# Optimization experiments

Hardware: AMD Instinct MI355X
Metric: run time of the kernel (lower is better)

The kernel has to match this reference:

```python
import jax, jax.numpy as jnp
import numpy as np

MODEL_DIM = 1024
N_HEADS = 16
HEAD_DIM = 64  # q_dim == k_dim == v_dim


def setup_inputs() -> dict:
    key = jax.random.key(0)
    ks = jax.random.split(key, 7)
    B, S = 4, 2048
    scale = 1.0 / np.sqrt(MODEL_DIM)
    return {
        "q": jax.random.normal(ks[0], (B, S, MODEL_DIM), dtype=jnp.float32),
        "k": jax.random.normal(ks[1], (B, S, MODEL_DIM), dtype=jnp.float32),
        "v": jax.random.normal(ks[2], (B, S, MODEL_DIM), dtype=jnp.float32),
        # Linear weights stored as [out, in] like torch; no biases.
        "wq": jax.random.normal(ks[3], (N_HEADS * HEAD_DIM, MODEL_DIM), dtype=jnp.float32) * scale,
        "wk": jax.random.normal(ks[4], (N_HEADS * HEAD_DIM, MODEL_DIM), dtype=jnp.float32) * scale,
        "wv": jax.random.normal(ks[5], (N_HEADS * HEAD_DIM, MODEL_DIM), dtype=jnp.float32) * scale,
        "wo": jax.random.normal(ks[6], (MODEL_DIM, N_HEADS * HEAD_DIM), dtype=jnp.float32) * scale,
    }


def reference(q, k, v, wq, wk, wv, wo):
    B, Sq, _ = q.shape
    Sk = k.shape[1]
    # projections: [B,S,D] @ W^T -> [B,S,H*dh] -> [B,H,S,dh]
    qh = (q @ wq.T).reshape(B, Sq, N_HEADS, HEAD_DIM).transpose(0, 2, 1, 3)
    kh = (k @ wk.T).reshape(B, Sk, N_HEADS, HEAD_DIM).transpose(0, 2, 1, 3)
    vh = (v @ wv.T).reshape(B, Sk, N_HEADS, HEAD_DIM).transpose(0, 2, 1, 3)
    # scores [B,H,Sq,Sk], scaled by sqrt(k_dim)
    scores = jnp.einsum('bhqd,bhkd->bhqk', qh, kh) / jnp.sqrt(jnp.float32(HEAD_DIM))
    attn = jax.nn.softmax(scores, axis=-1)
    ctx = jnp.einsum('bhqk,bhkd->bhqd', attn, vh)  # [B,H,Sq,dh]
    ctx = ctx.transpose(0, 2, 1, 3).reshape(B, Sq, N_HEADS * HEAD_DIM)
    return ctx @ wo.T
```

## Files before the change

### kernel.cpp

```cpp
#include <hip/hip_runtime.h>
#include <cstdint>
#include <cstddef>


typedef _Float16 f16x8 __attribute__((ext_vector_type(8)));
typedef _Float16 f16x4 __attribute__((ext_vector_type(4)));
typedef _Float16 f16x2 __attribute__((ext_vector_type(2)));
typedef __fp16 h16x2 __attribute__((ext_vector_type(2)));
typedef float f32x4 __attribute__((ext_vector_type(4)));
typedef float f32x16 __attribute__((ext_vector_type(16)));
typedef unsigned u32x4 __attribute__((ext_vector_type(4)));
typedef int i32x2 __attribute__((ext_vector_type(2)));

#define LDS_CAST(p) ((__attribute__((address_space(3))) void*)(p))
#define GLB_CAST(p) ((const __attribute__((address_space(1))) void*)(p))

__device__ __forceinline__ void gload_lds16(const void* g, void* l) {
  __builtin_amdgcn_global_load_lds(GLB_CAST(g), LDS_CAST(l), 16, 0, 0);
}

__device__ __forceinline__ float fexp2(float x) {
#if __has_builtin(__builtin_amdgcn_exp2f)
  return __builtin_amdgcn_exp2f(x);
#else
  return exp2f(x);
#endif
}

__device__ __forceinline__ f16x2 pkrtz(float a, float b) {
  h16x2 r = __builtin_amdgcn_cvt_pkrtz(a, b);
  return __builtin_bit_cast(f16x2, r);
}

__device__ __forceinline__ float dot2acc(f16x2 a, float acc) {
#if __has_builtin(__builtin_amdgcn_fdot2)
  const f16x2 one2 = {(_Float16)1.0f, (_Float16)1.0f};
  return __builtin_amdgcn_fdot2(a, one2, acc, false);
#else
  return acc + (float)a[0] + (float)a[1];
#endif
}

__device__ __forceinline__ void pl32swap(unsigned& a, unsigned& b) {
#if __has_builtin(__builtin_amdgcn_permlane32_swap)
  i32x2 r = __builtin_amdgcn_permlane32_swap((int)a, (int)b, false, false);
  a = (unsigned)r[0];
  b = (unsigned)r[1];
#else
  asm("v_permlane32_swap_b32 %0, %1" : "+v"(a), "+v"(b));
#endif
}

__global__ void cvt_all(const float* __restrict__ q, const float* __restrict__ k,
                        const float* __restrict__ v, const float* __restrict__ wq,
                        const float* __restrict__ wk, const float* __restrict__ wv,
                        const float* __restrict__ wo, _Float16* __restrict__ oq,
                        _Float16* __restrict__ ok, _Float16* __restrict__ ov,
                        _Float16* __restrict__ owq, _Float16* __restrict__ owk,
                        _Float16* __restrict__ owv, _Float16* __restrict__ owo) {
  int id = blockIdx.x;
  const float* in;
  _Float16* out;
  int base;
  if (id < 24576) {
    int z = id >> 13;
    base = (id & 8191) * 256;
    in = z == 0 ? q : z == 1 ? k : v;
    out = z == 0 ? oq : z == 1 ? ok : ov;
  } else {
    int id2 = id - 24576;
    int z = id2 >> 10;
    base = (id2 & 1023) * 256;
    in = z == 0 ? wq : z == 1 ? wk : z == 2 ? wv : wo;
    out = z == 0 ? owq : z == 1 ? owk : z == 2 ? owv : owo;
  }
  int i = base + threadIdx.x;
  float4 vv = ((const float4*)in)[i];
  f16x4 o = {(_Float16)vv.x, (_Float16)vv.y, (_Float16)vv.z, (_Float16)vv.w};
  ((f16x4*)out)[i] = o;
}

template <int MODE>
__device__ __forceinline__ void gemm_core(const _Float16* __restrict__ A,
                                          const _Float16* __restrict__ W,
                                          void* __restrict__ C, float scale,
                                          _Float16* As, _Float16* Bs) {
  constexpr int K = 1024, N = 1024;
  const int tid = threadIdx.x;
  const int wid = tid >> 6;
  const int lane = tid & 63;
  const int quad = lane >> 4;
  const int l16 = lane & 15;
  const int wm = wid >> 1;
  const int wn = wid & 1;

  int lin = blockIdx.y * 8 + blockIdx.x;
  int swz = (lin & 7) * 64 + (lin >> 3);
  const int m0 = (swz >> 3) * 128;
  const int n0 = (swz & 7) * 128;

  const _Float16* Ag = A + (size_t)m0 * K;
  const _Float16* Bg = W + (size_t)n0 * K;

  f32x4 acc[4][4];
#pragma unroll
  for (int i = 0; i < 4; i++)
#pragma unroll
    for (int j = 0; j < 4; j++) acc[i][j] = (f32x4){0.f, 0.f, 0.f, 0.f};

  const int lrow = lane >> 2;
  const int swsrc = ((lane & 3) ^ ((lane >> 3) & 3)) * 8;

  auto stage = [&](_Float16* Ad, _Float16* Bd, int k0) {
#pragma unroll
    for (int i = 0; i < 2; i++) {
      int issue = wid * 2 + i;
      gload_lds16(Ag + (size_t)(issue * 16 + lrow) * K + k0 + swsrc,
                  Ad + issue * 512);
      gload_lds16(Bg + (size_t)(issue * 16 + lrow) * K + k0 + swsrc,
                  Bd + issue * 512);
    }
  };

  const int swq = (quad ^ ((l16 >> 1) & 3)) * 8;

  auto compute = [&](const _Float16* Ab, const _Float16* Bb) {
    f16x8 af[4], bfr[4];
#pragma unroll
    for (int mt = 0; mt < 4; mt++)
      af[mt] = *(const f16x8*)&Ab[(wm * 64 + mt * 16 + l16) * 32 + swq];
#pragma unroll
    for (int nt = 0; nt < 4; nt++)
      bfr[nt] = *(const f16x8*)&Bb[(wn * 64 + nt * 16 + l16) * 32 + swq];
#pragma unroll
    for (int mt = 0; mt < 4; mt++)
#pragma unroll
      for (int nt = 0; nt < 4; nt++)
        acc[mt][nt] = __builtin_amdgcn_mfma_f32_16x16x32_f16(
            af[mt], bfr[nt], acc[mt][nt], 0, 0, 0);
  };

  _Float16* A0 = As;
  _Float16* A1 = As + 4096;
  _Float16* A2 = As + 8192;
  _Float16* B0 = Bs;
  _Float16* B1 = Bs + 4096;
  _Float16* B2 = Bs + 8192;

  stage(A0, B0, 0);
  for (int g = 0; g < 10; g++) {
    int t3 = g * 3;
    stage(A1, B1, (t3 + 1) * 32);
    asm volatile("s_waitcnt vmcnt(4)" ::: "memory");
    __builtin_amdgcn_s_barrier();
    asm volatile("" ::: "memory");
    compute(A0, B0);
    stage(A2, B2, (t3 + 2) * 32);
    asm volatile("s_waitcnt vmcnt(4)" ::: "memory");
    __builtin_amdgcn_s_barrier();
    asm volatile("" ::: "memory");
    compute(A1, B1);
    stage(A0, B0, (t3 + 3) * 32);
    asm volatile("s_waitcnt vmcnt(4)" ::: "memory");
    __builtin_amdgcn_s_barrier();
    asm volatile("" ::: "memory");
    compute(A2, B2);
  }
  stage(A1, B1, 31 * 32);
  asm volatile("s_waitcnt vmcnt(4)" ::: "memory");
  __builtin_amdgcn_s_barrier();
  asm volatile("" ::: "memory");
  compute(A0, B0);
  asm volatile("s_waitcnt vmcnt(0)" ::: "memory");
  __builtin_amdgcn_s_barrier();
  asm volatile("" ::: "memory");
  compute(A1, B1);

#pragma unroll
  for (int mt = 0; mt < 4; mt++) {
#pragma unroll
    for (int nt = 0; nt < 4; nt++) {
#pragma unroll
      for (int r = 0; r < 4; r++) {
        int m = m0 + wm * 64 + mt * 16 + quad * 4 + r;
        int n = n0 + wn * 64 + nt * 16 + l16;
        float v = acc[mt][nt][r] * scale;
        if (MODE == 0) {
          ((float*)C)[(size_t)m * N + n] = v;
        } else {
          int b = m >> 11, s = m & 2047;
          int h = n >> 6, dd = n & 63;
          size_t bh = (size_t)(b * 16 + h);
          if (MODE == 1) {
            ((_Float16*)C)[(bh * 2048 + s) * 64 + dd] = (_Float16)v;
          } else if (MODE == 3) {
            int kt2 = s >> 5, l32k = s & 31;
            int s4 = dd >> 4, hi8 = (dd >> 3) & 1, j = dd & 7;
            size_t idx = (bh * 32 + (kt2 >> 1)) * 8192 +
                         (((kt2 & 1) * 4 + s4) * 512) + (hi8 * 32 + l32k) * 8 +
                         j;
            ((_Float16*)C)[idx] = (_Float16)v;
          } else {
            int kt = s >> 6, ks = (s >> 4) & 3, hi8 = (s >> 3) & 1, j = s & 7;
            int dt = dd >> 5, l32v = dd & 31;
            size_t idx = (bh * 32 + kt) * 8192 + 4096 + ((dt * 4 + ks) * 512) +
                         (hi8 * 32 + l32v) * 8 + j;
            ((_Float16*)C)[idx] = (_Float16)v;
          }
        }
      }
    }
  }
}

__global__ __launch_bounds__(256, 3) void gemm_qkv(
    const _Float16* __restrict__ qb, const _Float16* __restrict__ kb,
    const _Float16* __restrict__ vb, const _Float16* __restrict__ wq,
    const _Float16* __restrict__ wk, const _Float16* __restrict__ wv,
    _Float16* __restrict__ Qh, _Float16* __restrict__ KVf) {
  __shared__ _Float16 As[3 * 128 * 32];
  __shared__ _Float16 Bs[3 * 128 * 32];
  if (blockIdx.z == 0)
    gemm_core<1>(qb, wq, Qh, 0.18033688f, As, Bs);
  else if (blockIdx.z == 1)
    gemm_core<3>(kb, wk, KVf, 1.0f, As, Bs);
  else
    gemm_core<4>(vb, wv, KVf, 1.0f, As, Bs);
}

__global__ __launch_bounds__(256, 3) void gemm_wo(
    const _Float16* __restrict__ ctx, const _Float16* __restrict__ wo,
    float* __restrict__ out) {
  __shared__ _Float16 As[3 * 128 * 32];
  __shared__ _Float16 Bs[3 * 128 * 32];
  gemm_core<0>(ctx, wo, out, 1.0f, As, Bs);
}

__global__ __launch_bounds__(512, 2) void attn_kernel(
    const _Float16* __restrict__ Qh, const _Float16* __restrict__ KVf,
    _Float16* __restrict__ ctx) {
  __shared__ _Float16 sKV[3][8192];

  const int qt = blockIdx.x;
  const int bh = blockIdx.y;
  const int tid = threadIdx.x;
  const int wid = tid >> 6;
  const int lane = tid & 63;
  const int l32 = lane & 31;
  const int hi = lane >> 5;

  const _Float16* Qg = Qh + ((size_t)bh * 2048 + qt * 256 + wid * 32) * 64;
  const _Float16* KVb = KVf + (size_t)bh * 262144;

  f16x8 aq[4];
#pragma unroll
  for (int s = 0; s < 4; s++)
    aq[s] = *(const f16x8*)(Qg + (size_t)l32 * 64 + s * 16 + hi * 8);

  f32x16 acc[2];
#pragma unroll
  for (int i = 0; i < 16; i++) {
    acc[0][i] = 0.f;
    acc[1][i] = 0.f;
  }
  float lsA = 0.f, lsB = 0.f;

  auto stage = [&](int buf, int kt) {
    const _Float16* t = KVb + (size_t)kt * 8192;
#pragma unroll
    for (int i = 0; i < 2; i++) {
      int c = wid * 2 + i;
      gload_lds16(t + c * 512 + lane * 8, &sKV[buf][c * 512]);
    }
  };

  auto body = [&](const _Float16* Ks) {
    const _Float16* Vs = Ks + 4096;
    f16x8 kf0[4], kf1[4];
#pragma unroll
    for (int s = 0; s < 4; s++) {
      kf0[s] = *(const f16x8*)&Ks[(0 * 4 + s) * 512 + lane * 8];
      kf1[s] = *(const f16x8*)&Ks[(4 + s) * 512 + lane * 8];
    }

    f32x16 s0, s1;
#pragma unroll
    for (int i = 0; i < 16; i++) {
      s0[i] = 0.f;
      s1[i] = 0.f;
    }
#pragma unroll
    for (int s = 0; s < 4; s++) {
      s0 = __builtin_amdgcn_mfma_f32_32x32x16_f16(kf0[s], aq[s], s0, 0, 0, 0);
      s1 = __builtin_amdgcn_mfma_f32_32x32x16_f16(kf1[s], aq[s], s1, 0, 0, 0);
    }

    f16x8 vf0[4], vf1[4];
#pragma unroll
    for (int g = 0; g < 4; g++) {
      vf0[g] = *(const f16x8*)&Vs[(0 * 4 + g) * 512 + lane * 8];
      vf1[g] = *(const f16x8*)&Vs[(4 + g) * 512 + lane * 8];
    }

    unsigned hw[2][8];
#pragma unroll
    for (int i = 0; i < 8; i++) {
      f16x2 hh = pkrtz(fexp2(s0[2 * i]), fexp2(s0[2 * i + 1]));
      if (i & 1)
        lsB = dot2acc(hh, lsB);
      else
        lsA = dot2acc(hh, lsA);
      hw[0][i] = __builtin_bit_cast(unsigned, hh);
    }
#pragma unroll
    for (int i = 0; i < 8; i++) {
      f16x2 hh = pkrtz(fexp2(s1[2 * i]), fexp2(s1[2 * i + 1]));
      if (i & 1)
        lsB = dot2acc(hh, lsB);
      else
        lsA = dot2acc(hh, lsA);
      hw[1][i] = __builtin_bit_cast(unsigned, hh);
    }

#pragma unroll
    for (int st = 0; st < 2; st++)
#pragma unroll
      for (int kh = 0; kh < 2; kh++) {
        unsigned w0 = hw[st][4 * kh + 0], w2 = hw[st][4 * kh + 2];
        unsigned w1 = hw[st][4 * kh + 1], w3 = hw[st][4 * kh + 3];
        pl32swap(w0, w2);
        pl32swap(w1, w3);
        u32x4 wv4 = {w0, w1, w2, w3};
        f16x8 pfrag = __builtin_bit_cast(f16x8, wv4);
        int g = st * 2 + kh;
        acc[0] = __builtin_amdgcn_mfma_f32_32x32x16_f16(vf0[g], pfrag, acc[0],
                                                        0, 0, 0);
        acc[1] = __builtin_amdgcn_mfma_f32_32x32x16_f16(vf1[g], pfrag, acc[1],
                                                        0, 0, 0);
      }
  };

  stage(0, 0);
  stage(1, 1);
  int cur = 0;

  for (int kt = 0; kt < 32; kt++) {
    if (kt < 31)
      asm volatile("s_waitcnt vmcnt(2)" ::: "memory");
    else
      asm volatile("s_waitcnt vmcnt(0)" ::: "memory");
    __builtin_amdgcn_s_barrier();
    asm volatile("" ::: "memory");

    if (kt < 30) {
      int sb = cur + 2;
      if (sb >= 3) sb -= 3;
      stage(sb, kt + 2);
    }

    body(sKV[cur]);

    cur = (cur == 2) ? 0 : cur + 1;
  }

  float lsum = lsA + lsB;
  float l = lsum + __shfl_xor(lsum, 32);
  float inv = 1.f / l;
  const int b = bh >> 4, h = bh & 15;
  int q = qt * 256 + wid * 32 + l32;
  _Float16* outp = ctx + ((size_t)b * 2048 + q) * 1024 + h * 64;
#pragma unroll
  for (int dt = 0; dt < 2; dt++)
#pragma unroll
    for (int g = 0; g < 4; g++) {
      f16x4 o;
#pragma unroll
      for (int c = 0; c < 4; c++) o[c] = (_Float16)(acc[dt][g * 4 + c] * inv);
      *(f16x4*)(outp + dt * 32 + g * 8 + hi * 4) = o;
    }
}

extern "C" void kernel_launch(void* const* d_in, const int* in_sizes, int n_in,
                              void* d_out, int out_size, void* d_ws,
                              size_t ws_size, hipStream_t stream) {
  const float* q = (const float*)d_in[0];
  const float* k = (const float*)d_in[1];
  const float* v = (const float*)d_in[2];
  const float* wq = (const float*)d_in[3];
  const float* wk = (const float*)d_in[4];
  const float* wv = (const float*)d_in[5];
  const float* wo = (const float*)d_in[6];
  float* out = (float*)d_out;

  const size_t SD = (size_t)8192 * 1024;
  const size_t WSZ = (size_t)1024 * 1024;

  _Float16* ws = (_Float16*)d_ws;
  _Float16* qb = ws;
  _Float16* kb = ws + 1 * SD;
  _Float16* vb = ws + 2 * SD;
  _Float16* Qh = ws + 3 * SD;
  _Float16* KVf = ws + 4 * SD;
  _Float16* ctx = ws + 6 * SD;
  _Float16* wqb = ws + 7 * SD;
  _Float16* wkb = wqb + WSZ;
  _Float16* wvb = wqb + 2 * WSZ;
  _Float16* wob = wqb + 3 * WSZ;

  cvt_all<<<dim3(28672), 256, 0, stream>>>(q, k, v, wq, wk, wv, wo, qb, kb, vb,
                                           wqb, wkb, wvb, wob);

  gemm_qkv<<<dim3(8, 64, 3), 256, 0, stream>>>(qb, kb, vb, wqb, wkb, wvb, Qh,
                                               KVf);

  attn_kernel<<<dim3(8, 64), 512, 0, stream>>>(Qh, KVf, ctx);

  gemm_wo<<<dim3(8, 64), 256, 0, stream>>>(ctx, wob, out);
}
```

Measured before the change: 320.1 us.

## Double-buffer KV tiles in pairs to halve attention loop barriers

The attention kernel's KV pipeline changes from a 3-slot ring with one barrier per tile to a 4-slot scheme that loads and processes two tiles per barrier phase. The aim is to halve the number of s_waitcnt/s_barrier synchronisations and drop the modulo-3 buffer indexing. In exchange, LDS per block grows from 48KB to 64KB. With 2 blocks per CU that reaches 128KB, which may limit occupancy. The prefetch distance within each pair is also uneven.

```diff
diff --git a/kernel.cpp b/kernel.cpp
--- a/kernel.cpp
+++ b/kernel.cpp
@@ -239,7 +239,7 @@
 __global__ __launch_bounds__(512, 2) void attn_kernel(
     const _Float16* __restrict__ Qh, const _Float16* __restrict__ KVf,
     _Float16* __restrict__ ctx) {
-  __shared__ _Float16 sKV[3][8192];
+  __shared__ _Float16 sKV[4][8192];
 
   const int qt = blockIdx.x;
   const int bh = blockIdx.y;
@@ -342,26 +342,36 @@
 
   stage(0, 0);
   stage(1, 1);
-  int cur = 0;
-
-  for (int kt = 0; kt < 32; kt++) {
-    if (kt < 31)
-      asm volatile("s_waitcnt vmcnt(2)" ::: "memory");
-    else
-      asm volatile("s_waitcnt vmcnt(0)" ::: "memory");
+
+  for (int gg = 0; gg < 7; gg++) {
+    int t = gg * 4;
+    asm volatile("s_waitcnt vmcnt(0)" ::: "memory");
     __builtin_amdgcn_s_barrier();
     asm volatile("" ::: "memory");
-
-    if (kt < 30) {
-      int sb = cur + 2;
-      if (sb >= 3) sb -= 3;
-      stage(sb, kt + 2);
-    }
-
-    body(sKV[cur]);
-
-    cur = (cur == 2) ? 0 : cur + 1;
+    stage(2, t + 2);
+    stage(3, t + 3);
+    body(sKV[0]);
+    body(sKV[1]);
+    asm volatile("s_waitcnt vmcnt(0)" ::: "memory");
+    __builtin_amdgcn_s_barrier();
+    asm volatile("" ::: "memory");
+    stage(0, t + 4);
+    stage(1, t + 5);
+    body(sKV[2]);
+    body(sKV[3]);
   }
+  asm volatile("s_waitcnt vmcnt(0)" ::: "memory");
+  __builtin_amdgcn_s_barrier();
+  asm volatile("" ::: "memory");
+  stage(2, 30);
+  stage(3, 31);
+  body(sKV[0]);
+  body(sKV[1]);
+  asm volatile("s_waitcnt vmcnt(0)" ::: "memory");
+  __builtin_amdgcn_s_barrier();
+  asm volatile("" ::: "memory");
+  body(sKV[2]);
+  body(sKV[3]);
 
   float lsum = lsA + lsB;
   float l = lsum + __shfl_xor(lsum, 32);
```

Result: no change. 322.6 us (+0.8%).
